# Optimization experiments

Hardware: AMD Instinct MI355X
Metric: run time of the kernel (lower is better)

Reference implementation:

```python
import jax, jax.numpy as jnp
import numpy as np

B, T = 32, 1024
IN0 = 512   # 2 * hidden_dim
H = 256     # input_dim // 2


def _lstm_layer(x, Wih, Whh, bih, bhh):
    """Single unidirectional LSTM layer, PyTorch gate order (i, f, g, o).
    x: [B, T, D] -> returns h sequence [B, T, H]."""
    # Precompute the input projection for all timesteps in one big GEMM.
    xg = jnp.einsum('btd,gd->btg', x, Wih) + bih + bhh  # [B, T, 4H]
    xg = jnp.swapaxes(xg, 0, 1)                          # [T, B, 4H]

    h0 = jnp.zeros((x.shape[0], H), x.dtype)
    c0 = jnp.zeros((x.shape[0], H), x.dtype)

    def step(carry, xg_t):
        h, c = carry
        gates = xg_t + h @ Whh.T            # [B, 4H]
        i, f, g, o = jnp.split(gates, 4, axis=-1)
        i = jax.nn.sigmoid(i)
        f = jax.nn.sigmoid(f)
        g = jnp.tanh(g)
        o = jax.nn.sigmoid(o)
        c = f * c + i * g
        h = o * jnp.tanh(c)
        return (h, c), h

    (_, _), hs = jax.lax.scan(step, (h0, c0), xg)  # hs: [T, B, H]
    return jnp.swapaxes(hs, 0, 1)                  # [B, T, H]


def setup_inputs() -> dict:
    key = jax.random.key(0)
    ks = jax.random.split(key, 9)
    s = 1.0 / np.sqrt(H)  # torch LSTM init scale
    u = lambda k, shp: jax.random.uniform(k, shp, jnp.float32, -s, s)
    return {
        'encoder_outputs': jax.random.normal(ks[0], (B, T, IN0), jnp.float32),
        'Wih0': u(ks[1], (4 * H, IN0)),
        'Whh0': u(ks[2], (4 * H, H)),
        'bih0': u(ks[3], (4 * H,)),
        'bhh0': u(ks[4], (4 * H,)),
        'Wih1': u(ks[5], (4 * H, H)),
        'Whh1': u(ks[6], (4 * H, H)),
        'bih1': u(ks[7], (4 * H,)),
        'bhh1': u(ks[8], (4 * H,)),
    }


def reference(encoder_outputs, Wih0, Whh0, bih0, bhh0, Wih1, Whh1, bih1, bhh1):
    h1 = _lstm_layer(encoder_outputs, Wih0, Whh0, bih0, bhh0)
    # dropout=0.0 between layers (eval-mode math)
    h2 = _lstm_layer(h1, Wih1, Whh1, bih1, bhh1)
    return h2  # [B, T, H] reconstruction
```

## Files before the change

### kernel.cpp

```cpp
#include <hip/hip_runtime.h>

#define BATCH 32
#define TFULL 1024
#define HDIM  256
#define G4    1024
#define TC    128
#define NWG   512

__global__ __launch_bounds__(512) void gemm_xg(
    const float* __restrict__ X, const float* __restrict__ W,
    const float* __restrict__ bia, const float* __restrict__ bib,
    float* __restrict__ xg, int K, int trows, int t0)
{
  __shared__ float Xs[16][128];
  __shared__ float Ws[16][128];
  const int tid = threadIdx.x;
  const int m0 = blockIdx.x * 128;
  const int n0 = blockIdx.y * 128;
  const int tx = tid & 15;
  const int ty = tid >> 4;

  float acc[4][8];
#pragma unroll
  for (int i = 0; i < 4; ++i)
#pragma unroll
    for (int j = 0; j < 8; ++j) acc[i][j] = 0.f;

  const int r  = tid >> 2;
  const int kq = tid & 3;
  const int m  = m0 + r;
  const int bX = m & 31;
  const int tl = m >> 5;
  const float* xrow = X + (bX * trows + t0 + tl) * K;
  const float* wrow = W + (n0 + r) * K;

  for (int kt = 0; kt < K; kt += 16) {
    float4 xv = *(const float4*)&xrow[kt + kq * 4];
    float4 wv = *(const float4*)&wrow[kt + kq * 4];
    Xs[kq * 4 + 0][r] = xv.x; Xs[kq * 4 + 1][r] = xv.y;
    Xs[kq * 4 + 2][r] = xv.z; Xs[kq * 4 + 3][r] = xv.w;
    Ws[kq * 4 + 0][r] = wv.x; Ws[kq * 4 + 1][r] = wv.y;
    Ws[kq * 4 + 2][r] = wv.z; Ws[kq * 4 + 3][r] = wv.w;
    __syncthreads();
#pragma unroll
    for (int k = 0; k < 16; ++k) {
      float4 xa = *(const float4*)&Xs[k][ty * 4];
      float4 wa = *(const float4*)&Ws[k][tx * 8];
      float4 wb = *(const float4*)&Ws[k][tx * 8 + 4];
      float xr[4] = {xa.x, xa.y, xa.z, xa.w};
      float wr[8] = {wa.x, wa.y, wa.z, wa.w, wb.x, wb.y, wb.z, wb.w};
#pragma unroll
      for (int i = 0; i < 4; ++i)
#pragma unroll
        for (int j = 0; j < 8; ++j)
          acc[i][j] = fmaf(xr[i], wr[j], acc[i][j]);
    }
    __syncthreads();
  }

  float bb[8];
#pragma unroll
  for (int j = 0; j < 8; ++j) {
    int n = n0 + tx * 8 + j;
    bb[j] = bia[n] + bib[n];
  }
#pragma unroll
  for (int i = 0; i < 4; ++i) {
    int mm = m0 + ty * 4 + i;
    int b = mm & 31, t = mm >> 5;
    float* dst = &xg[(size_t)(t * BATCH + b) * G4 + n0 + tx * 8];
    float4 v0 = make_float4(acc[i][0] + bb[0], acc[i][1] + bb[1],
                            acc[i][2] + bb[2], acc[i][3] + bb[3]);
    float4 v1 = make_float4(acc[i][4] + bb[4], acc[i][5] + bb[5],
                            acc[i][6] + bb[6], acc[i][7] + bb[7]);
    *(float4*)dst = v0;
    *(float4*)(dst + 4) = v1;
  }
}

#define PIN_LOAD8(A,B,C,D,E,F,G,H, PTR)                                \
  asm volatile(                                                        \
      "global_load_dwordx4 %0, %8, off\n\t"                            \
      "global_load_dwordx4 %1, %8, off offset:16\n\t"                  \
      "global_load_dwordx4 %2, %8, off offset:32\n\t"                  \
      "global_load_dwordx4 %3, %8, off offset:48\n\t"                  \
      "global_load_dwordx4 %4, %8, off offset:64\n\t"                  \
      "global_load_dwordx4 %5, %8, off offset:80\n\t"                  \
      "global_load_dwordx4 %6, %8, off offset:96\n\t"                  \
      "global_load_dwordx4 %7, %8, off offset:112\n\t"                 \
      "s_waitcnt vmcnt(0)"                                             \
      : "=&v"(A), "=&v"(B), "=&v"(C), "=&v"(D),                        \
        "=&v"(E), "=&v"(F), "=&v"(G), "=&v"(H)                         \
      : "v"(PTR) : "memory")

#define FMA4(ACC, WV, HV)                                              \
  ACC = fmaf((WV).x, (HV).x, ACC); ACC = fmaf((WV).y, (HV).y, ACC);    \
  ACC = fmaf((WV).z, (HV).z, ACC); ACC = fmaf((WV).w, (HV).w, ACC)

#define DOT16(ACC, W, HP)                                              \
  FMA4(ACC, W##0, (HP)[0]);  FMA4(ACC, W##1, (HP)[1]);                 \
  FMA4(ACC, W##2, (HP)[2]);  FMA4(ACC, W##3, (HP)[3]);                 \
  FMA4(ACC, W##4, (HP)[4]);  FMA4(ACC, W##5, (HP)[5]);                 \
  FMA4(ACC, W##6, (HP)[6]);  FMA4(ACC, W##7, (HP)[7]);                 \
  FMA4(ACC, W##8, (HP)[8]);  FMA4(ACC, W##9, (HP)[9]);                 \
  FMA4(ACC, W##a, (HP)[10]); FMA4(ACC, W##b, (HP)[11]);                \
  FMA4(ACC, W##c, (HP)[12]); FMA4(ACC, W##d, (HP)[13]);                \
  FMA4(ACC, W##e, (HP)[14]); FMA4(ACC, W##f, (HP)[15])

__device__ __forceinline__ float sigm_f(float x) {
  return 1.f / (1.f + __expf(-x));
}
__device__ __forceinline__ float tanh_f(float x) {
  return 1.f - 2.f / (1.f + __expf(2.f * x));
}

__global__ __launch_bounds__(256, 2) void lstm_scan2(
    const float* __restrict__ xg0,
    const float* __restrict__ Whh0,
    const float* __restrict__ Wih1,
    const float* __restrict__ Whh1,
    const float* __restrict__ bih1, const float* __restrict__ bhh1,
    float* __restrict__ out,
    float* __restrict__ mbA,
    float* __restrict__ mbB,
    float* __restrict__ cbA,
    float* __restrict__ cbB,
    int T0, int niter, int nL0)
{
  const int w    = blockIdx.x;
  const int tid  = threadIdx.x;
  const int s    = w & 31;
  const int r    = w >> 5;
  const int gt   = tid >> 6;
  const int lane = tid & 63;
  const int jl   = lane & 15;
  const int kq   = lane >> 4;
  const int n    = gt * 256 + r * 16 + jl;
  const int swz  = tid & 15;

  __shared__ __align__(16) float wi_lds[256 * 64];
  __shared__ __align__(16) float hAq[4 * 68];
  __shared__ __align__(16) float hBq[4 * 68];
  __shared__ float part0[64];
  __shared__ float part1[64];

  {
    const float4* src = (const float4*)(Wih1 + (size_t)n * HDIM + kq * 64);
    float* wb = &wi_lds[tid * 64];
#pragma unroll
    for (int q = 0; q < 16; ++q)
      *(float4*)&wb[(q ^ swz) << 2] = src[q];
  }

  float4 w00,w01,w02,w03,w04,w05,w06,w07,w08,w09,w0a,w0b,w0c,w0d,w0e,w0f;
  float4 w10,w11,w12,w13,w14,w15,w16,w17,w18,w19,w1a,w1b,w1c,w1d,w1e,w1f;
  {
    const float4* p0 = (const float4*)(Whh0 + (size_t)n * HDIM + kq * 64);
    const float4* p1 = (const float4*)(Whh1 + (size_t)n * HDIM + kq * 64);
    PIN_LOAD8(w00,w01,w02,w03,w04,w05,w06,w07, p0);
    PIN_LOAD8(w08,w09,w0a,w0b,w0c,w0d,w0e,w0f, p0 + 8);
    PIN_LOAD8(w10,w11,w12,w13,w14,w15,w16,w17, p1);
    PIN_LOAD8(w18,w19,w1a,w1b,w1c,w1d,w1e,w1f, p1 + 8);
  }
  const float bs1 = bih1[n] + bhh1[n];

  float cA = 0.f, cB = 0.f;
  if (tid < 16)              cA = cbA[s * HDIM + r * 16 + tid];
  if (tid >= 64 && tid < 80) cB = cbB[s * HDIM + r * 16 + (tid - 64)];

  float* mA = mbA + (size_t)s * 8 * 512;
  float* mB = mbB + (size_t)s * 8 * 512;
  __syncthreads();

  for (int i = 0; i < niter; ++i) {
    const int t = T0 + i;
    const bool doL0 = (i < nL0);
    const bool doL1 = (t > 0);
    const unsigned gA = (unsigned)t;
    const unsigned gB = (unsigned)(t - 1);

    float xv = 0.f;
    if (doL0 && lane < 16) xv = xg0[((size_t)(i * BATCH + s) << 10) + n];

    unsigned long long bp0 = 0, bp1 = 0, bp2 = 0, bp3 = 0;
    if (doL1 && tid >= 64 && tid < 128) {
      const unsigned long long* bp =
          (const unsigned long long*)(mB + (size_t)(gB & 7) * 512) +
          (size_t)(tid - 64) * 4;
      bp0 = __hip_atomic_load(bp + 0, __ATOMIC_RELAXED, __HIP_MEMORY_SCOPE_AGENT);
      bp1 = __hip_atomic_load(bp + 1, __ATOMIC_RELAXED, __HIP_MEMORY_SCOPE_AGENT);
      bp2 = __hip_atomic_load(bp + 2, __ATOMIC_RELAXED, __HIP_MEMORY_SCOPE_AGENT);
      bp3 = __hip_atomic_load(bp + 3, __ATOMIC_RELAXED, __HIP_MEMORY_SCOPE_AGENT);
    }

    if (tid < 64) {
      const float4* sp = (const float4*)(mA + (size_t)(gA & 7) * 512) + tid * 2;
      float4 A, B;
      for (;;) {
        asm volatile(
            "global_load_dwordx4 %0, %2, off sc0 sc1\n\t"
            "global_load_dwordx4 %1, %3, off sc0 sc1\n\t"
            "s_waitcnt vmcnt(0)"
            : "=&v"(A), "=&v"(B) : "v"(sp), "v"(sp + 1) : "memory");
        bool ok = (__float_as_uint(A.y) == gA) && (__float_as_uint(A.w) == gA) &&
                  (__float_as_uint(B.y) == gA) && (__float_as_uint(B.w) == gA);
        if (__all(ok)) break;
      }
      *(float4*)&hAq[(tid >> 4) * 68 + ((4 * tid) & 63)] =
          make_float4(A.x, A.z, B.x, B.z);
    }
    __syncthreads();

    if (doL0) {
      const float4* hp = (const float4*)&hAq[kq * 68];
      float a = 0.f;
      DOT16(a, w0, hp);
      a += __shfl_xor(a, 16);
      a += __shfl_xor(a, 32);
      if (lane < 16) part0[gt * 16 + jl] = a + xv;
    }
    __syncthreads();

    if (doL0 && tid < 16) {
      float ig = sigm_f(part0[tid]);
      float fg = sigm_f(part0[16 + tid]);
      float gv = tanh_f(part0[32 + tid]);
      float og = sigm_f(part0[48 + tid]);
      cA = fg * cA + ig * gv;
      float h = og * tanh_f(cA);
      unsigned long long pv =
          ((unsigned long long)(gA + 1u) << 32) |
          (unsigned long long)__float_as_uint(h);
      unsigned long long* pp =
          (unsigned long long*)(mA + (size_t)((gA + 1u) & 7) * 512) +
          (r * 16 + tid);
      __hip_atomic_store(pp, pv, __ATOMIC_RELAXED, __HIP_MEMORY_SCOPE_AGENT);
    }

    if (doL1 && tid >= 64 && tid < 128) {
      const int l2 = tid - 64;
      float h0, h1, h2, h3;
      bool ok = ((unsigned)(bp0 >> 32) == gB) && ((unsigned)(bp1 >> 32) == gB) &&
                ((unsigned)(bp2 >> 32) == gB) && ((unsigned)(bp3 >> 32) == gB);
      if (__all(ok)) {
        h0 = __uint_as_float((unsigned)bp0);
        h1 = __uint_as_float((unsigned)bp1);
        h2 = __uint_as_float((unsigned)bp2);
        h3 = __uint_as_float((unsigned)bp3);
      } else {
        const float4* sp = (const float4*)(mB + (size_t)(gB & 7) * 512) + l2 * 2;
        float4 A, B;
        for (;;) {
          asm volatile(
              "global_load_dwordx4 %0, %2, off sc0 sc1\n\t"
              "global_load_dwordx4 %1, %3, off sc0 sc1\n\t"
              "s_waitcnt vmcnt(0)"
              : "=&v"(A), "=&v"(B) : "v"(sp), "v"(sp + 1) : "memory");
          bool ok2 = (__float_as_uint(A.y) == gB) && (__float_as_uint(A.w) == gB) &&
                     (__float_as_uint(B.y) == gB) && (__float_as_uint(B.w) == gB);
          if (__all(ok2)) break;
        }
        h0 = A.x; h1 = A.z; h2 = B.x; h3 = B.z;
      }
      *(float4*)&hBq[(l2 >> 4) * 68 + ((4 * l2) & 63)] =
          make_float4(h0, h1, h2, h3);
    }
    __syncthreads();

    if (doL1) {
      const float4* ha = (const float4*)&hAq[kq * 68];
      const float4* hb = (const float4*)&hBq[kq * 68];
      const float* wb = &wi_lds[tid * 64];
      float u = 0.f, v = 0.f;
#pragma unroll
      for (int q = 0; q < 16; ++q) {
        float4 wv = *(const float4*)&wb[(q ^ swz) << 2];
        FMA4(u, wv, ha[q]);
      }
      DOT16(v, w1, hb);
      float a = u + v;
      a += __shfl_xor(a, 16);
      a += __shfl_xor(a, 32);
      if (lane < 16) part1[gt * 16 + jl] = a + bs1;
    }
    __syncthreads();

    if (doL1 && tid >= 64 && tid < 80) {
      const int l = tid - 64;
      float ig = sigm_f(part1[l]);
      float fg = sigm_f(part1[16 + l]);
      float gv = tanh_f(part1[32 + l]);
      float og = sigm_f(part1[48 + l]);
      cB = fg * cB + ig * gv;
      float h = og * tanh_f(cB);
      unsigned long long pv =
          ((unsigned long long)gA << 32) |
          (unsigned long long)__float_as_uint(h);
      unsigned long long* pp =
          (unsigned long long*)(mB + (size_t)(gA & 7) * 512) + (r * 16 + l);
      __hip_atomic_store(pp, pv, __ATOMIC_RELAXED, __HIP_MEMORY_SCOPE_AGENT);
      out[((size_t)s * TFULL + (t - 1)) * HDIM + r * 16 + l] = h;
    }
  }

  if (tid < 16)              cbA[s * HDIM + r * 16 + tid] = cA;
  if (tid >= 64 && tid < 80) cbB[s * HDIM + r * 16 + (tid - 64)] = cB;
}

extern "C" void kernel_launch(void* const* d_in, const int* in_sizes, int n_in,
                              void* d_out, int out_size, void* d_ws, size_t ws_size,
                              hipStream_t stream) {
  (void)in_sizes; (void)n_in; (void)out_size; (void)ws_size;
  const float* enc  = (const float*)d_in[0];
  const float* Wih0 = (const float*)d_in[1];
  const float* Whh0 = (const float*)d_in[2];
  const float* bih0 = (const float*)d_in[3];
  const float* bhh0 = (const float*)d_in[4];
  const float* Wih1 = (const float*)d_in[5];
  const float* Whh1 = (const float*)d_in[6];
  const float* bih1 = (const float*)d_in[7];
  const float* bhh1 = (const float*)d_in[8];
  float* out = (float*)d_out;

  float* ws  = (float*)d_ws;
  float* xg  = ws;
  float* st  = ws + 4194304;
  float* mbA = st;
  float* mbB = st + 131072;
  float* cbA = st + 262144;
  float* cbB = st + 270336;

  hipMemsetAsync(st, 0, (size_t)278528 * 4, stream);

  for (int ch = 0; ch < 8; ++ch) {
    gemm_xg<<<dim3(32, 8), 512, 0, stream>>>(enc, Wih0, bih0, bhh0, xg,
                                             512, TFULL, ch * TC);
    lstm_scan2<<<NWG, 256, 0, stream>>>(xg, Whh0, Wih1, Whh1, bih1, bhh1,
                                        out, mbA, mbB, cbA, cbB,
                                        ch * TC, (ch == 7) ? TC + 1 : TC, TC);
  }
}
```

Measured before the change: 2.988 ms.

## Skew layer-1 LSTM two steps behind layer 0 to overlap cross-block polling

Restructures the fused two-layer scan so layer 1 runs two timesteps behind layer 0 instead of one. Layer-1 work now consumes a double-buffered copy of the layer-0 hidden state from the previous iteration. The layer-0 poll is issued early and checked after layer-1 compute, which hides the global-memory handshake latency behind the layer-1 dot products. The cost is an extra prologue read of the prior chunk's state, one more tail iteration, and more complex step/tag indexing that must stay consistent across chunk launches.

```diff
diff --git a/kernel.cpp b/kernel.cpp
--- a/kernel.cpp
+++ b/kernel.cpp
@@ -139,8 +139,8 @@
   const int swz  = tid & 15;
 
   __shared__ __align__(16) float wi_lds[256 * 64];
-  __shared__ __align__(16) float hAq[4 * 68];
-  __shared__ __align__(16) float hBq[4 * 68];
+  __shared__ __align__(16) float hAq[2][272];
+  __shared__ __align__(16) float hBq[272];
   __shared__ float part0[64];
   __shared__ float part1[64];
 
@@ -170,83 +170,66 @@
 
   float* mA = mbA + (size_t)s * 8 * 512;
   float* mB = mbB + (size_t)s * 8 * 512;
+
+  if (T0 >= 2 && tid < 64) {
+    const unsigned gP = (unsigned)(T0 - 1);
+    const float4* sp = (const float4*)(mA + (size_t)(gP & 7) * 512) + tid * 2;
+    float4 A, B;
+    for (;;) {
+      asm volatile(
+          "global_load_dwordx4 %0, %2, off sc0 sc1\n\t"
+          "global_load_dwordx4 %1, %3, off sc0 sc1\n\t"
+          "s_waitcnt vmcnt(0)"
+          : "=&v"(A), "=&v"(B) : "v"(sp), "v"(sp + 1) : "memory");
+      bool ok = (__float_as_uint(A.y) == gP) && (__float_as_uint(A.w) == gP) &&
+                (__float_as_uint(B.y) == gP) && (__float_as_uint(B.w) == gP);
+      if (__all(ok)) break;
+    }
+    *(float4*)&hAq[1][(tid >> 4) * 68 + ((4 * tid) & 63)] =
+        make_float4(A.x, A.z, B.x, B.z);
+  }
   __syncthreads();
 
   for (int i = 0; i < niter; ++i) {
     const int t = T0 + i;
-    const bool doL0 = (i < nL0);
-    const bool doL1 = (t > 0);
+    const bool doL0   = (i < nL0);
+    const bool doPoll = (i <= nL0);
+    const bool doL1   = (t >= 2);
+    const int  cur    = i & 1;
     const unsigned gA = (unsigned)t;
-    const unsigned gB = (unsigned)(t - 1);
+    const unsigned gB = (unsigned)(t - 2);
 
     float xv = 0.f;
     if (doL0 && lane < 16) xv = xg0[((size_t)(i * BATCH + s) << 10) + n];
 
-    unsigned long long bp0 = 0, bp1 = 0, bp2 = 0, bp3 = 0;
+    unsigned long long ap0 = 0, ap1 = 0, ap2 = 0, ap3 = 0;
+    if (doPoll && tid < 64) {
+      const unsigned long long* ap =
+          (const unsigned long long*)(mA + (size_t)(gA & 7) * 512) +
+          (size_t)tid * 4;
+      ap0 = __hip_atomic_load(ap + 0, __ATOMIC_RELAXED, __HIP_MEMORY_SCOPE_AGENT);
+      ap1 = __hip_atomic_load(ap + 1, __ATOMIC_RELAXED, __HIP_MEMORY_SCOPE_AGENT);
+      ap2 = __hip_atomic_load(ap + 2, __ATOMIC_RELAXED, __HIP_MEMORY_SCOPE_AGENT);
+      ap3 = __hip_atomic_load(ap + 3, __ATOMIC_RELAXED, __HIP_MEMORY_SCOPE_AGENT);
+    }
+
     if (doL1 && tid >= 64 && tid < 128) {
+      const int l2 = tid - 64;
       const unsigned long long* bp =
           (const unsigned long long*)(mB + (size_t)(gB & 7) * 512) +
-          (size_t)(tid - 64) * 4;
-      bp0 = __hip_atomic_load(bp + 0, __ATOMIC_RELAXED, __HIP_MEMORY_SCOPE_AGENT);
-      bp1 = __hip_atomic_load(bp + 1, __ATOMIC_RELAXED, __HIP_MEMORY_SCOPE_AGENT);
-      bp2 = __hip_atomic_load(bp + 2, __ATOMIC_RELAXED, __HIP_MEMORY_SCOPE_AGENT);
-      bp3 = __hip_atomic_load(bp + 3, __ATOMIC_RELAXED, __HIP_MEMORY_SCOPE_AGENT);
-    }
-
-    if (tid < 64) {
-      const float4* sp = (const float4*)(mA + (size_t)(gA & 7) * 512) + tid * 2;
-      float4 A, B;
-      for (;;) {
-        asm volatile(
-            "global_load_dwordx4 %0, %2, off sc0 sc1\n\t"
-            "global_load_dwordx4 %1, %3, off sc0 sc1\n\t"
-            "s_waitcnt vmcnt(0)"
-            : "=&v"(A), "=&v"(B) : "v"(sp), "v"(sp + 1) : "memory");
-        bool ok = (__float_as_uint(A.y) == gA) && (__float_as_uint(A.w) == gA) &&
-                  (__float_as_uint(B.y) == gA) && (__float_as_uint(B.w) == gA);
-        if (__all(ok)) break;
-      }
-      *(float4*)&hAq[(tid >> 4) * 68 + ((4 * tid) & 63)] =
-          make_float4(A.x, A.z, B.x, B.z);
-    }
-    __syncthreads();
-
-    if (doL0) {
-      const float4* hp = (const float4*)&hAq[kq * 68];
-      float a = 0.f;
-      DOT16(a, w0, hp);
-      a += __shfl_xor(a, 16);
-      a += __shfl_xor(a, 32);
-      if (lane < 16) part0[gt * 16 + jl] = a + xv;
-    }
-    __syncthreads();
-
-    if (doL0 && tid < 16) {
-      float ig = sigm_f(part0[tid]);
-      float fg = sigm_f(part0[16 + tid]);
-      float gv = tanh_f(part0[32 + tid]);
-      float og = sigm_f(part0[48 + tid]);
-      cA = fg * cA + ig * gv;
-      float h = og * tanh_f(cA);
-      unsigned long long pv =
-          ((unsigned long long)(gA + 1u) << 32) |
-          (unsigned long long)__float_as_uint(h);
-      unsigned long long* pp =
-          (unsigned long long*)(mA + (size_t)((gA + 1u) & 7) * 512) +
-          (r * 16 + tid);
-      __hip_atomic_store(pp, pv, __ATOMIC_RELAXED, __HIP_MEMORY_SCOPE_AGENT);
-    }
-
-    if (doL1 && tid >= 64 && tid < 128) {
-      const int l2 = tid - 64;
+          (size_t)l2 * 4;
+      unsigned long long b0 = __hip_atomic_load(bp + 0, __ATOMIC_RELAXED, __HIP_MEMORY_SCOPE_AGENT);
+      unsigned long long b1 = __hip_atomic_load(bp + 1, __ATOMIC_RELAXED, __HIP_MEMORY_SCOPE_AGENT);
+      unsigned long long b2 = __hip_atomic_load(bp + 2, __ATOMIC_RELAXED, __HIP_MEMORY_SCOPE_AGENT);
+      unsigned long long b3 = __hip_atomic_load(bp + 3, __ATOMIC_RELAXED, __HIP_MEMORY_SCOPE_AGENT);
       float h0, h1, h2, h3;
-      bool ok = ((unsigned)(bp0 >> 32) == gB) && ((unsigned)(bp1 >> 32) == gB) &&
-                ((unsigned)(bp2 >> 32) == gB) && ((unsigned)(bp3 >> 32) == gB);
+      bool ok = ((unsigned)(b0 >> 32) == gB) && ((unsigned)(b1 >> 32) == gB) &&
+                ((unsigned)(b2 >> 32) == gB) && ((unsigned)(b3 >> 32) == gB);
       if (__all(ok)) {
-        h0 = __uint_as_float((unsigned)bp0);
-        h1 = __uint_as_float((unsigned)bp1);
-        h2 = __uint_as_float((unsigned)bp2);
-        h3 = __uint_as_float((unsigned)bp3);
+        h0 = __uint_as_float((unsigned)b0);
+        h1 = __uint_as_float((unsigned)b1);
+        h2 = __uint_as_float((unsigned)b2);
+        h3 = __uint_as_float((unsigned)b3);
       } else {
         const float4* sp = (const float4*)(mB + (size_t)(gB & 7) * 512) + l2 * 2;
         float4 A, B;
@@ -268,7 +251,7 @@
     __syncthreads();
 
     if (doL1) {
-      const float4* ha = (const float4*)&hAq[kq * 68];
+      const float4* ha = (const float4*)&hAq[cur ^ 1][kq * 68];
       const float4* hb = (const float4*)&hBq[kq * 68];
       const float* wb = &wi_lds[tid * 64];
       float u = 0.f, v = 0.f;
@@ -294,12 +277,67 @@
       cB = fg * cB + ig * gv;
       float h = og * tanh_f(cB);
       unsigned long long pv =
-          ((unsigned long long)gA << 32) |
+          ((unsigned long long)(unsigned)(t - 1) << 32) |
           (unsigned long long)__float_as_uint(h);
       unsigned long long* pp =
-          (unsigned long long*)(mB + (size_t)(gA & 7) * 512) + (r * 16 + l);
+          (unsigned long long*)(mB + (size_t)((t - 1) & 7) * 512) +
+          (r * 16 + l);
       __hip_atomic_store(pp, pv, __ATOMIC_RELAXED, __HIP_MEMORY_SCOPE_AGENT);
-      out[((size_t)s * TFULL + (t - 1)) * HDIM + r * 16 + l] = h;
+      out[((size_t)s * TFULL + (t - 2)) * HDIM + r * 16 + l] = h;
+    }
+    if (doPoll && tid < 64) {
+      float h0, h1, h2, h3;
+      bool ok = ((unsigned)(ap0 >> 32) == gA) && ((unsigned)(ap1 >> 32) == gA) &&
+                ((unsigned)(ap2 >> 32) == gA) && ((unsigned)(ap3 >> 32) == gA);
+      if (__all(ok)) {
+        h0 = __uint_as_float((unsigned)ap0);
+        h1 = __uint_as_float((unsigned)ap1);
+        h2 = __uint_as_float((unsigned)ap2);
+        h3 = __uint_as_float((unsigned)ap3);
+      } else {
+        const float4* sp = (const float4*)(mA + (size_t)(gA & 7) * 512) + tid * 2;
+        float4 A, B;
+        for (;;) {
+          asm volatile(
+              "global_load_dwordx4 %0, %2, off sc0 sc1\n\t"
+              "global_load_dwordx4 %1, %3, off sc0 sc1\n\t"
+              "s_waitcnt vmcnt(0)"
+              : "=&v"(A), "=&v"(B) : "v"(sp), "v"(sp + 1) : "memory");
+          bool ok2 = (__float_as_uint(A.y) == gA) && (__float_as_uint(A.w) == gA) &&
+                     (__float_as_uint(B.y) == gA) && (__float_as_uint(B.w) == gA);
+          if (__all(ok2)) break;
+        }
+        h0 = A.x; h1 = A.z; h2 = B.x; h3 = B.z;
+      }
+      *(float4*)&hAq[cur][(tid >> 4) * 68 + ((4 * tid) & 63)] =
+          make_float4(h0, h1, h2, h3);
+    }
+    __syncthreads();
+
+    if (doL0) {
+      const float4* hp = (const float4*)&hAq[cur][kq * 68];
+      float a = 0.f;
+      DOT16(a, w0, hp);
+      a += __shfl_xor(a, 16);
+      a += __shfl_xor(a, 32);
+      if (lane < 16) part0[gt * 16 + jl] = a + xv;
+    }
+    __syncthreads();
+
+    if (doL0 && tid < 16) {
+      float ig = sigm_f(part0[tid]);
+      float fg = sigm_f(part0[16 + tid]);
+      float gv = tanh_f(part0[32 + tid]);
+      float og = sigm_f(part0[48 + tid]);
+      cA = fg * cA + ig * gv;
+      float h = og * tanh_f(cA);
+      unsigned long long pv =
+          ((unsigned long long)(gA + 1u) << 32) |
+          (unsigned long long)__float_as_uint(h);
+      unsigned long long* pp =
+          (unsigned long long*)(mA + (size_t)((gA + 1u) & 7) * 512) +
+          (r * 16 + tid);
+      __hip_atomic_store(pp, pv, __ATOMIC_RELAXED, __HIP_MEMORY_SCOPE_AGENT);
     }
   }
 
@@ -337,6 +375,6 @@
                                              512, TFULL, ch * TC);
     lstm_scan2<<<NWG, 256, 0, stream>>>(xg, Whh0, Wih1, Whh1, bih1, bhh1,
                                         out, mbA, mbB, cbA, cbB,
-                                        ch * TC, (ch == 7) ? TC + 1 : TC, TC);
-  }
-}
+                                        ch * TC, (ch == 7) ? TC + 2 : TC, TC);
+  }
+}
```

Measured after the change: 3.017 ms. About the same (+1.0%).
